# Kernel tuning notes

Measured on AMD Instinct MI355X. Metric: run time of the kernel, lower is better.

Reference implementation:

```python
import jax, jax.numpy as jnp
import numpy as np

T = 10
EPS = 1e-05
NUM_CHANNELS = 64  # d: whitening block size per group


def setup_inputs() -> dict:
    key = jax.random.key(0)
    X = jax.random.normal(key, (64, 256, 56, 56), dtype=jnp.float32)
    weight = jnp.ones((1, 256, 1, 1), dtype=jnp.float32)
    bias = jnp.zeros((1, 256, 1, 1), dtype=jnp.float32)
    return {"X": X, "weight": weight, "bias": bias}


def reference(X, weight, bias):
    N, C, H, W = X.shape
    d = NUM_CHANNELS
    g = C // d
    # [N,C,H,W] -> [C,N,H,W] -> (g, d, m)
    x = jnp.transpose(X, (1, 0, 2, 3)).reshape(g, d, -1)
    m = x.shape[-1]
    mean = jnp.mean(x, axis=-1, keepdims=True)          # (g, d, 1)
    xc = x - mean
    I = jnp.eye(d, dtype=X.dtype)
    # Sigma = eps*I + xc xc^T / m
    Sigma = EPS * I + jnp.einsum('gdm,gem->gde', xc, xc) / m
    rTr = 1.0 / jnp.trace(Sigma, axis1=1, axis2=2)[:, None, None]  # (g,1,1)
    Sigma_N = Sigma * rTr
    P0 = jnp.broadcast_to(I, (g, d, d))

    def newton_step(P, _):
        P3 = jnp.matmul(jnp.matmul(P, P), P)
        return 1.5 * P - 0.5 * jnp.matmul(P3, Sigma_N), None

    P, _ = jax.lax.scan(newton_step, P0, None, length=T)
    wm = P * jnp.sqrt(rTr)                               # (g, d, d)
    xn = jnp.matmul(wm, xc)                              # (g, d, m)
    X_hat = jnp.transpose(xn.reshape(C, N, H, W), (1, 0, 2, 3))
    return X_hat * weight + bias
```

## Files before the change

kernel.cpp:

```cpp
#include <hip/hip_runtime.h>


#define HWSZ 3136
#define CCH 256
#define DCH 64
#define MTOT (64 * HWSZ)
#define EPSV 1e-5f
#define TST 68
#define NST 68

typedef __attribute__((ext_vector_type(8))) short short8v;
typedef __attribute__((ext_vector_type(4))) float floatx4;

union F8U {
  short8v v;
  unsigned u[4];
  uint2 u2[2];
};

__device__ __forceinline__ unsigned short f2bf(float f) {
  unsigned u = __float_as_uint(f);
  u += 0x7fffu + ((u >> 16) & 1u);
  return (unsigned short)(u >> 16);
}
__device__ __forceinline__ float bf2f(unsigned short h) {
  return __uint_as_float(((unsigned)h) << 16);
}

__device__ __forceinline__ void sync_lds() {
  asm volatile("s_waitcnt lgkmcnt(0)\n\ts_barrier" ::: "memory");
}

__global__ __launch_bounds__(256) void cov_kernel(const float* __restrict__ X,
                                                  float* __restrict__ cov_dst,
                                                  float* __restrict__ sum_dst, int use_part) {
  __shared__ unsigned short tile[64 * TST];
  int bid = blockIdx.x;
  int g = bid >> 8;
  int nn = (bid >> 2) & 63;
  int qh = bid & 3;
  int ks0 = (qh * 49) >> 2;
  int ks1 = ((qh + 1) * 49) >> 2;
  int tid = threadIdx.x;
  int c = tid >> 2, q = tid & 3;
  int w = tid >> 6, lane = tid & 63, quad = lane >> 4, lm = lane & 15;

  floatx4 acc[4];
#pragma unroll
  for (int tj = 0; tj < 4; tj++) {
    floatx4 z = {0.f, 0.f, 0.f, 0.f};
    acc[tj] = z;
  }
  float fsum = 0.f;

  const float* xbase = X + ((size_t)(nn * CCH + g * DCH + c)) * HWSZ;

  float4 v[4];
  {
    int k0 = ks0 * 64;
#pragma unroll
    for (int j = 0; j < 4; j++) v[j] = *(const float4*)(xbase + k0 + j * 16 + q * 4);
  }

  for (int ks = ks0; ks < ks1; ks++) {
#pragma unroll
    for (int j = 0; j < 4; j++) {
      float4 t = v[j];
      fsum += t.x + t.y + t.z + t.w;
      unsigned d0 = (unsigned)f2bf(t.x) | ((unsigned)f2bf(t.y) << 16);
      unsigned d1 = (unsigned)f2bf(t.z) | ((unsigned)f2bf(t.w) << 16);
      *(uint2*)&tile[c * TST + j * 16 + q * 4] = make_uint2(d0, d1);
    }
    sync_lds();
    if (ks + 1 < ks1) {
      int k0 = (ks + 1) * 64;
#pragma unroll
      for (int j = 0; j < 4; j++) v[j] = *(const float4*)(xbase + k0 + j * 16 + q * 4);
    }
#pragma unroll
    for (int kk = 0; kk < 2; kk++) {
      F8U a;
      a.u2[0] = *(const uint2*)&tile[(16 * w + lm) * TST + kk * 32 + quad * 8];
      a.u2[1] = *(const uint2*)&tile[(16 * w + lm) * TST + kk * 32 + quad * 8 + 4];
#pragma unroll
      for (int tj = 0; tj < 4; tj++) {
        F8U b;
        b.u2[0] = *(const uint2*)&tile[(16 * tj + lm) * TST + kk * 32 + quad * 8];
        b.u2[1] = *(const uint2*)&tile[(16 * tj + lm) * TST + kk * 32 + quad * 8 + 4];
        acc[tj] = __builtin_amdgcn_mfma_f32_16x16x32_bf16(a.v, b.v, acc[tj], 0, 0, 0);
      }
    }
    sync_lds();
  }

  int pidx = bid & 255;
  if (use_part) {
    float* dst = cov_dst + ((size_t)g * 256 + pidx) * 4096;
#pragma unroll
    for (int tj = 0; tj < 4; tj++)
#pragma unroll
      for (int rr = 0; rr < 4; rr++)
        dst[(16 * w + quad * 4 + rr) * 64 + 16 * tj + lm] = acc[tj][rr];
  } else {
    float* dst = cov_dst + (size_t)g * 4096;
#pragma unroll
    for (int tj = 0; tj < 4; tj++)
#pragma unroll
      for (int rr = 0; rr < 4; rr++)
        atomicAdd(&dst[(16 * w + quad * 4 + rr) * 64 + 16 * tj + lm], acc[tj][rr]);
  }

  fsum += __shfl_xor(fsum, 1);
  fsum += __shfl_xor(fsum, 2);
  if (q == 0) {
    if (use_part)
      sum_dst[((size_t)g * 256 + pidx) * 64 + c] = fsum;
    else
      atomicAdd(&sum_dst[g * 64 + c], fsum);
  }
}

__global__ __launch_bounds__(256) void mean_kernel(const float* __restrict__ sum_part,
                                                   float* __restrict__ meanWS, int npart) {
  __shared__ float red[256];
  int g = blockIdx.x, tid = threadIdx.x;
  int c = tid & 63, p0 = tid >> 6;
  float s0 = 0.f, s1 = 0.f;
  for (int p = p0; p + 4 < npart; p += 8) {
    s0 += sum_part[((size_t)g * npart + p) * 64 + c];
    s1 += sum_part[((size_t)g * npart + p + 4) * 64 + c];
  }
  for (int p = p0 + ((npart - p0 + 7) / 8) * 8 - 8 + 8; p < npart; p += 4) s0 += 0.f;
  if (((npart >> 2) & 1) && (p0 + ((npart >> 2) - 1) * 4 < npart)) {
    int p = ((npart >> 2) - 1) * 4 + p0;
    if (p < npart) s0 += sum_part[((size_t)g * npart + p) * 64 + c];
  }
  red[tid] = s0 + s1;
  __syncthreads();
  if (tid < 64)
    meanWS[g * 64 + tid] =
        (red[tid] + red[tid + 64] + red[tid + 128] + red[tid + 192]) / (float)MTOT;
}

__global__ __launch_bounds__(256) void sigma_kernel(const float* __restrict__ cov_part,
                                                    const float* __restrict__ meanWS,
                                                    float* __restrict__ Sigma, int npart) {
  __shared__ float red[256];
  int b = blockIdx.x;
  int g = b >> 6, r = b & 63;
  int tid = threadIdx.x;
  int e = tid & 63, p0 = tid >> 6;
  float s = 0.f;
  for (int p = p0; p < npart; p += 4)
    s += cov_part[((size_t)g * npart + p) * 4096 + r * 64 + e];
  red[tid] = s;
  __syncthreads();
  if (tid < 64) {
    float tot = red[tid] + red[tid + 64] + red[tid + 128] + red[tid + 192];
    float mr = meanWS[g * 64 + r], me = meanWS[g * 64 + tid];
    Sigma[(size_t)g * 4096 + r * 64 + tid] =
        tot / (float)MTOT - mr * me + (r == tid ? EPSV : 0.f);
  }
}

__device__ __forceinline__ void mm_planes(floatx4 acc[4], const unsigned short* Ah,
                                          const unsigned short* Al, const unsigned short* Bh,
                                          const unsigned short* Bl, int w, int quad, int lm) {
#pragma unroll
  for (int tj = 0; tj < 4; tj++) {
    floatx4 z = {0.f, 0.f, 0.f, 0.f};
    acc[tj] = z;
  }
#pragma unroll
  for (int kk = 0; kk < 2; kk++) {
    int abase = (16 * w + lm) * NST + kk * 32 + quad * 8;
    F8U ahi, alo;
    ahi.u2[0] = *(const uint2*)&Ah[abase];
    ahi.u2[1] = *(const uint2*)&Ah[abase + 4];
    alo.u2[0] = *(const uint2*)&Al[abase];
    alo.u2[1] = *(const uint2*)&Al[abase + 4];
#pragma unroll
    for (int tj = 0; tj < 4; tj++) {
      int bbase = (16 * tj + lm) * NST + kk * 32 + quad * 8;
      F8U bhi, blo;
      bhi.u2[0] = *(const uint2*)&Bh[bbase];
      bhi.u2[1] = *(const uint2*)&Bh[bbase + 4];
      blo.u2[0] = *(const uint2*)&Bl[bbase];
      blo.u2[1] = *(const uint2*)&Bl[bbase + 4];
      acc[tj] = __builtin_amdgcn_mfma_f32_16x16x32_bf16(ahi.v, bhi.v, acc[tj], 0, 0, 0);
      acc[tj] = __builtin_amdgcn_mfma_f32_16x16x32_bf16(ahi.v, blo.v, acc[tj], 0, 0, 0);
      acc[tj] = __builtin_amdgcn_mfma_f32_16x16x32_bf16(alo.v, bhi.v, acc[tj], 0, 0, 0);
    }
  }
}

__device__ __forceinline__ void store_tr(const floatx4 acc[4], unsigned short* H,
                                         unsigned short* L, int w, int quad, int lm) {
#pragma unroll
  for (int tj = 0; tj < 4; tj++) {
    unsigned short hs[4], ls[4];
#pragma unroll
    for (int rr = 0; rr < 4; rr++) {
      float f = acc[tj][rr];
      hs[rr] = f2bf(f);
      ls[rr] = f2bf(f - bf2f(hs[rr]));
    }
    int a = (16 * tj + lm) * NST + 16 * w + quad * 4;
    *(uint2*)&H[a] = make_uint2((unsigned)hs[0] | ((unsigned)hs[1] << 16),
                                (unsigned)hs[2] | ((unsigned)hs[3] << 16));
    *(uint2*)&L[a] = make_uint2((unsigned)ls[0] | ((unsigned)ls[1] << 16),
                                (unsigned)ls[2] | ((unsigned)ls[3] << 16));
  }
}

__global__ __launch_bounds__(256) void newton_kernel(const float* __restrict__ Sigma,
                                                     unsigned short* __restrict__ wmB) {
  __shared__ unsigned short Ph[64 * NST], Pl[64 * NST];
  __shared__ unsigned short Sh[64 * NST], Sl[64 * NST];
  __shared__ unsigned short Th[64 * NST], Tl[64 * NST];
  __shared__ unsigned short Uh[64 * NST], Ul[64 * NST];
  __shared__ float diag[64];
  int g = blockIdx.x, tid = threadIdx.x;
  int w = tid >> 6, lane = tid & 63, quad = lane >> 4, lm = lane & 15;
  const float* Sg = Sigma + (size_t)g * 4096;

  if (tid < 64) diag[tid] = Sg[tid * 65];
  __syncthreads();
  float tr = 0.f;
#pragma unroll 8
  for (int i = 0; i < 64; i++) tr += diag[i];
  float rTr = 1.0f / tr;

  for (int idx = tid; idx < 4096; idx += 256) {
    int r = idx >> 6, c2 = idx & 63;
    float vv = Sg[idx] * rTr;
    unsigned short h = f2bf(vv);
    Sh[r * NST + c2] = h;
    Sl[r * NST + c2] = f2bf(vv - bf2f(h));
    Ph[r * NST + c2] = (r == c2) ? (unsigned short)0x3f80 : (unsigned short)0;
    Pl[r * NST + c2] = 0;
  }
  sync_lds();

  floatx4 acc[4];
  float pf[4][4];

  for (int t = 0; t < 10; t++) {
    mm_planes(acc, Ph, Pl, Ph, Pl, w, quad, lm);
    store_tr(acc, Th, Tl, w, quad, lm);
    sync_lds();
    mm_planes(acc, Th, Tl, Ph, Pl, w, quad, lm);
    store_tr(acc, Uh, Ul, w, quad, lm);
    sync_lds();
    mm_planes(acc, Uh, Ul, Sh, Sl, w, quad, lm);
#pragma unroll
    for (int tj = 0; tj < 4; tj++) {
      int a = (16 * tj + lm) * NST + 16 * w + quad * 4;
      uint2 ho = *(const uint2*)&Ph[a];
      uint2 lo = *(const uint2*)&Pl[a];
      unsigned short hs[4] = {(unsigned short)(ho.x & 0xffff), (unsigned short)(ho.x >> 16),
                              (unsigned short)(ho.y & 0xffff), (unsigned short)(ho.y >> 16)};
      unsigned short lss[4] = {(unsigned short)(lo.x & 0xffff), (unsigned short)(lo.x >> 16),
                               (unsigned short)(lo.y & 0xffff), (unsigned short)(lo.y >> 16)};
      unsigned short nh[4], nl[4];
#pragma unroll
      for (int rr = 0; rr < 4; rr++) {
        float pown = bf2f(hs[rr]) + bf2f(lss[rr]);
        float f = 1.5f * pown - 0.5f * acc[tj][rr];
        pf[tj][rr] = f;
        nh[rr] = f2bf(f);
        nl[rr] = f2bf(f - bf2f(nh[rr]));
      }
      *(uint2*)&Ph[a] = make_uint2((unsigned)nh[0] | ((unsigned)nh[1] << 16),
                                   (unsigned)nh[2] | ((unsigned)nh[3] << 16));
      *(uint2*)&Pl[a] = make_uint2((unsigned)nl[0] | ((unsigned)nl[1] << 16),
                                   (unsigned)nl[2] | ((unsigned)nl[3] << 16));
    }
    sync_lds();
  }

  float sc = sqrtf(rTr);
  unsigned short* wg = wmB + (size_t)g * 4096;
#pragma unroll
  for (int tj = 0; tj < 4; tj++)
#pragma unroll
    for (int rr = 0; rr < 4; rr++) {
      int row = 16 * w + quad * 4 + rr, col = 16 * tj + lm;
      wg[row * 64 + col] = f2bf(pf[tj][rr] * sc);
    }
}

__global__ __launch_bounds__(256) void apply_kernel(
    const float* __restrict__ X, const unsigned short* __restrict__ wmB,
    const float* __restrict__ meanWS, const float* __restrict__ weight,
    const float* __restrict__ bias, float* __restrict__ out) {
  __shared__ unsigned short T[64 * TST];
  __shared__ float meanv[64], wv[64], bv[64];
  int bid = blockIdx.x;
  int g = bid >> 8;
  int nn = (bid >> 2) & 63;
  int qh = bid & 3;
  int ks0 = (qh * 49) >> 2;
  int ks1 = ((qh + 1) * 49) >> 2;
  int tid = threadIdx.x;
  int w = tid >> 6, lane = tid & 63, quad = lane >> 4, lm = lane & 15;
  int sl = tid & 63;
  int cg = tid >> 6;

  if (tid < 64) {
    meanv[tid] = meanWS[g * 64 + tid];
    wv[tid] = weight[g * 64 + tid];
    bv[tid] = bias[g * 64 + tid];
  }
  F8U afrag[2];
#pragma unroll
  for (int kk = 0; kk < 2; kk++) {
    const uint2* p =
        (const uint2*)&wmB[(size_t)g * 4096 + (16 * w + lm) * 64 + kk * 32 + quad * 8];
    afrag[kk].u2[0] = p[0];
    afrag[kk].u2[1] = p[1];
  }
  __syncthreads();

  const float* xg = X + ((size_t)(nn * CCH + g * DCH)) * HWSZ;
  float* og = out + ((size_t)(nn * CCH + g * DCH)) * HWSZ;
  const float* xs = xg + (size_t)(cg * 16) * HWSZ + sl;

  float vv[16];
  {
    int k0 = ks0 * 64;
#pragma unroll
    for (int jp = 0; jp < 16; jp++) vv[jp] = xs[(size_t)jp * HWSZ + k0];
  }

  for (int ks = ks0; ks < ks1; ks++) {
    int k0 = ks * 64;
#pragma unroll
    for (int p2 = 0; p2 < 4; p2++) {
      unsigned d0 = (unsigned)f2bf(vv[4 * p2] - meanv[cg * 16 + 4 * p2]) |
                    ((unsigned)f2bf(vv[4 * p2 + 1] - meanv[cg * 16 + 4 * p2 + 1]) << 16);
      unsigned d1 = (unsigned)f2bf(vv[4 * p2 + 2] - meanv[cg * 16 + 4 * p2 + 2]) |
                    ((unsigned)f2bf(vv[4 * p2 + 3] - meanv[cg * 16 + 4 * p2 + 3]) << 16);
      *(uint2*)&T[sl * TST + cg * 16 + p2 * 4] = make_uint2(d0, d1);
    }
    sync_lds();
    if (ks + 1 < ks1) {
      int k0n = (ks + 1) * 64;
#pragma unroll
      for (int jp = 0; jp < 16; jp++) vv[jp] = xs[(size_t)jp * HWSZ + k0n];
    }
    floatx4 acc[4];
#pragma unroll
    for (int tj = 0; tj < 4; tj++) {
      floatx4 z = {0.f, 0.f, 0.f, 0.f};
      acc[tj] = z;
    }
#pragma unroll
    for (int kk = 0; kk < 2; kk++) {
#pragma unroll
      for (int tj = 0; tj < 4; tj++) {
        F8U b;
        b.u2[0] = *(const uint2*)&T[(16 * tj + lm) * TST + kk * 32 + quad * 8];
        b.u2[1] = *(const uint2*)&T[(16 * tj + lm) * TST + kk * 32 + quad * 8 + 4];
        acc[tj] = __builtin_amdgcn_mfma_f32_16x16x32_bf16(afrag[kk].v, b.v, acc[tj], 0, 0, 0);
      }
    }
#pragma unroll
    for (int tj = 0; tj < 4; tj++)
#pragma unroll
      for (int rr = 0; rr < 4; rr++) {
        int cc = 16 * w + quad * 4 + rr;
        og[(size_t)cc * HWSZ + k0 + 16 * tj + lm] = acc[tj][rr] * wv[cc] + bv[cc];
      }
    sync_lds();
  }
}

extern "C" void kernel_launch(void* const* d_in, const int* in_sizes, int n_in, void* d_out,
                              int out_size, void* d_ws, size_t ws_size, hipStream_t stream) {
  (void)in_sizes;
  (void)n_in;
  (void)out_size;
  const float* X = (const float*)d_in[0];
  const float* weight = (const float*)d_in[1];
  const float* bias = (const float*)d_in[2];
  float* out = (float*)d_out;
  char* ws = (char*)d_ws;

  float* Sigma = (float*)(ws + 0);
  float* meanWS = (float*)(ws + 65536);
  unsigned short* wmB = (unsigned short*)(ws + 66560);
  float* cov_dst = (float*)(ws + 99328);
  const size_t need_part = 99328u + 16777216u + 262144u;
  int use_part = (ws_size >= need_part) ? 1 : 0;
  float* sum_dst =
      use_part ? (float*)(ws + 99328 + 16777216) : (float*)(ws + 99328 + 65536);
  int npart = use_part ? 256 : 1;

  if (!use_part) {
    hipMemsetAsync(cov_dst, 0, 65536 + 1024, stream);
  }

  cov_kernel<<<dim3(1024), dim3(256), 0, stream>>>(X, cov_dst, sum_dst, use_part);
  mean_kernel<<<dim3(4), dim3(256), 0, stream>>>(sum_dst, meanWS, npart);
  sigma_kernel<<<dim3(256), dim3(256), 0, stream>>>(cov_dst, meanWS, Sigma, npart);
  newton_kernel<<<dim3(4), dim3(256), 0, stream>>>(Sigma, wmB);
  apply_kernel<<<dim3(1024), dim3(256), 0, stream>>>(X, wmB, meanWS, weight, bias, out);
}
```

Measured before the change: 453.6 us.

## Double-buffer LDS tiles, fuse mean into sigma kernel, widen Newton to 512 threads

The cov and apply kernels now use two LDS tile buffers, so each k-step needs one barrier instead of two and the next global load is issued before that barrier. The mean reduction moves into sigma_kernel, where every block recomputes the group mean from the partial sums; this removes one launch. The Newton kernel runs 8 waves, each computing half the column tiles, so the serial 64x64 iteration has more parallelism per block. The costs are double the LDS footprint and redundant mean reads in every sigma block.

```diff
diff --git a/kernel.cpp b/kernel.cpp
--- a/kernel.cpp
+++ b/kernel.cpp
@@ -34,7 +34,7 @@
 __global__ __launch_bounds__(256) void cov_kernel(const float* __restrict__ X,
                                                   float* __restrict__ cov_dst,
                                                   float* __restrict__ sum_dst, int use_part) {
-  __shared__ unsigned short tile[64 * TST];
+  __shared__ unsigned short tile[2][64 * TST];
   int bid = blockIdx.x;
   int g = bid >> 8;
   int nn = (bid >> 2) & 63;
@@ -62,6 +62,7 @@
     for (int j = 0; j < 4; j++) v[j] = *(const float4*)(xbase + k0 + j * 16 + q * 4);
   }
 
+  int p = 0;
   for (int ks = ks0; ks < ks1; ks++) {
 #pragma unroll
     for (int j = 0; j < 4; j++) {
@@ -69,28 +70,28 @@
       fsum += t.x + t.y + t.z + t.w;
       unsigned d0 = (unsigned)f2bf(t.x) | ((unsigned)f2bf(t.y) << 16);
       unsigned d1 = (unsigned)f2bf(t.z) | ((unsigned)f2bf(t.w) << 16);
-      *(uint2*)&tile[c * TST + j * 16 + q * 4] = make_uint2(d0, d1);
-    }
-    sync_lds();
+      *(uint2*)&tile[p][c * TST + j * 16 + q * 4] = make_uint2(d0, d1);
+    }
     if (ks + 1 < ks1) {
       int k0 = (ks + 1) * 64;
 #pragma unroll
       for (int j = 0; j < 4; j++) v[j] = *(const float4*)(xbase + k0 + j * 16 + q * 4);
     }
+    sync_lds();
 #pragma unroll
     for (int kk = 0; kk < 2; kk++) {
       F8U a;
-      a.u2[0] = *(const uint2*)&tile[(16 * w + lm) * TST + kk * 32 + quad * 8];
-      a.u2[1] = *(const uint2*)&tile[(16 * w + lm) * TST + kk * 32 + quad * 8 + 4];
+      a.u2[0] = *(const uint2*)&tile[p][(16 * w + lm) * TST + kk * 32 + quad * 8];
+      a.u2[1] = *(const uint2*)&tile[p][(16 * w + lm) * TST + kk * 32 + quad * 8 + 4];
 #pragma unroll
       for (int tj = 0; tj < 4; tj++) {
         F8U b;
-        b.u2[0] = *(const uint2*)&tile[(16 * tj + lm) * TST + kk * 32 + quad * 8];
-        b.u2[1] = *(const uint2*)&tile[(16 * tj + lm) * TST + kk * 32 + quad * 8 + 4];
+        b.u2[0] = *(const uint2*)&tile[p][(16 * tj + lm) * TST + kk * 32 + quad * 8];
+        b.u2[1] = *(const uint2*)&tile[p][(16 * tj + lm) * TST + kk * 32 + quad * 8 + 4];
         acc[tj] = __builtin_amdgcn_mfma_f32_16x16x32_bf16(a.v, b.v, acc[tj], 0, 0, 0);
       }
     }
-    sync_lds();
+    p ^= 1;
   }
 
   int pidx = bid & 255;
@@ -120,68 +121,60 @@
   }
 }
 
-__global__ __launch_bounds__(256) void mean_kernel(const float* __restrict__ sum_part,
-                                                   float* __restrict__ meanWS, int npart) {
+__global__ __launch_bounds__(256) void sigma_kernel(const float* __restrict__ cov_part,
+                                                    const float* __restrict__ sum_part,
+                                                    float* __restrict__ Sigma,
+                                                    float* __restrict__ meanWS, int npart) {
   __shared__ float red[256];
-  int g = blockIdx.x, tid = threadIdx.x;
-  int c = tid & 63, p0 = tid >> 6;
-  float s0 = 0.f, s1 = 0.f;
-  for (int p = p0; p + 4 < npart; p += 8) {
-    s0 += sum_part[((size_t)g * npart + p) * 64 + c];
-    s1 += sum_part[((size_t)g * npart + p + 4) * 64 + c];
-  }
-  for (int p = p0 + ((npart - p0 + 7) / 8) * 8 - 8 + 8; p < npart; p += 4) s0 += 0.f;
-  if (((npart >> 2) & 1) && (p0 + ((npart >> 2) - 1) * 4 < npart)) {
-    int p = ((npart >> 2) - 1) * 4 + p0;
-    if (p < npart) s0 += sum_part[((size_t)g * npart + p) * 64 + c];
-  }
-  red[tid] = s0 + s1;
-  __syncthreads();
-  if (tid < 64)
-    meanWS[g * 64 + tid] =
-        (red[tid] + red[tid + 64] + red[tid + 128] + red[tid + 192]) / (float)MTOT;
-}
-
-__global__ __launch_bounds__(256) void sigma_kernel(const float* __restrict__ cov_part,
-                                                    const float* __restrict__ meanWS,
-                                                    float* __restrict__ Sigma, int npart) {
-  __shared__ float red[256];
+  __shared__ float meanv[64];
   int b = blockIdx.x;
   int g = b >> 6, r = b & 63;
   int tid = threadIdx.x;
-  int e = tid & 63, p0 = tid >> 6;
+  int c = tid & 63, p0 = tid >> 6;
+
   float s = 0.f;
-  for (int p = p0; p < npart; p += 4)
-    s += cov_part[((size_t)g * npart + p) * 4096 + r * 64 + e];
+  for (int pp = p0; pp < npart; pp += 4)
+    s += sum_part[((size_t)g * npart + pp) * 64 + c];
   red[tid] = s;
+  __syncthreads();
+  if (tid < 64)
+    meanv[tid] = (red[tid] + red[tid + 64] + red[tid + 128] + red[tid + 192]) / (float)MTOT;
+
+  float s2 = 0.f;
+  for (int pp = p0; pp < npart; pp += 4)
+    s2 += cov_part[((size_t)g * npart + pp) * 4096 + r * 64 + c];
+  __syncthreads();
+  red[tid] = s2;
   __syncthreads();
   if (tid < 64) {
     float tot = red[tid] + red[tid + 64] + red[tid + 128] + red[tid + 192];
-    float mr = meanWS[g * 64 + r], me = meanWS[g * 64 + tid];
     Sigma[(size_t)g * 4096 + r * 64 + tid] =
-        tot / (float)MTOT - mr * me + (r == tid ? EPSV : 0.f);
-  }
-}
-
-__device__ __forceinline__ void mm_planes(floatx4 acc[4], const unsigned short* Ah,
+        tot / (float)MTOT - meanv[r] * meanv[tid] + (r == tid ? EPSV : 0.f);
+    if (r == 0) meanWS[g * 64 + tid] = meanv[tid];
+  }
+}
+
+__device__ __forceinline__ void mm_planes(floatx4 acc[2], const unsigned short* Ah,
                                           const unsigned short* Al, const unsigned short* Bh,
-                                          const unsigned short* Bl, int w, int quad, int lm) {
-#pragma unroll
-  for (int tj = 0; tj < 4; tj++) {
+                                          const unsigned short* Bl, int rw, int ch, int quad,
+                                          int lm) {
+#pragma unroll
+  for (int tj = 0; tj < 2; tj++) {
     floatx4 z = {0.f, 0.f, 0.f, 0.f};
     acc[tj] = z;
   }
 #pragma unroll
   for (int kk = 0; kk < 2; kk++) {
-    int abase = (16 * w + lm) * NST + kk * 32 + quad * 8;
+    int abase = (16 * rw + lm) * NST + kk * 32 + quad * 8;
     F8U ahi, alo;
     ahi.u2[0] = *(const uint2*)&Ah[abase];
     ahi.u2[1] = *(const uint2*)&Ah[abase + 4];
     alo.u2[0] = *(const uint2*)&Al[abase];
     alo.u2[1] = *(const uint2*)&Al[abase + 4];
 #pragma unroll
-    for (int tj = 0; tj < 4; tj++) {
-      int bbase = (16 * tj + lm) * NST + kk * 32 + quad * 8;
+    for (int tj = 0; tj < 2; tj++) {
+      int tjg = 2 * ch + tj;
+      int bbase = (16 * tjg + lm) * NST + kk * 32 + quad * 8;
       F8U bhi, blo;
       bhi.u2[0] = *(const uint2*)&Bh[bbase];
       bhi.u2[1] = *(const uint2*)&Bh[bbase + 4];
@@ -194,10 +187,11 @@
   }
 }
 
-__device__ __forceinline__ void store_tr(const floatx4 acc[4], unsigned short* H,
-                                         unsigned short* L, int w, int quad, int lm) {
-#pragma unroll
-  for (int tj = 0; tj < 4; tj++) {
+__device__ __forceinline__ void store_tr(const floatx4 acc[2], unsigned short* H,
+                                         unsigned short* L, int rw, int ch, int quad, int lm) {
+#pragma unroll
+  for (int tj = 0; tj < 2; tj++) {
+    int tjg = 2 * ch + tj;
     unsigned short hs[4], ls[4];
 #pragma unroll
     for (int rr = 0; rr < 4; rr++) {
@@ -205,7 +199,7 @@
       hs[rr] = f2bf(f);
       ls[rr] = f2bf(f - bf2f(hs[rr]));
     }
-    int a = (16 * tj + lm) * NST + 16 * w + quad * 4;
+    int a = (16 * tjg + lm) * NST + 16 * rw + quad * 4;
     *(uint2*)&H[a] = make_uint2((unsigned)hs[0] | ((unsigned)hs[1] << 16),
                                 (unsigned)hs[2] | ((unsigned)hs[3] << 16));
     *(uint2*)&L[a] = make_uint2((unsigned)ls[0] | ((unsigned)ls[1] << 16),
@@ -213,7 +207,7 @@
   }
 }
 
-__global__ __launch_bounds__(256) void newton_kernel(const float* __restrict__ Sigma,
+__global__ __launch_bounds__(512) void newton_kernel(const float* __restrict__ Sigma,
                                                      unsigned short* __restrict__ wmB) {
   __shared__ unsigned short Ph[64 * NST], Pl[64 * NST];
   __shared__ unsigned short Sh[64 * NST], Sl[64 * NST];
@@ -222,6 +216,7 @@
   __shared__ float diag[64];
   int g = blockIdx.x, tid = threadIdx.x;
   int w = tid >> 6, lane = tid & 63, quad = lane >> 4, lm = lane & 15;
+  int rw = w & 3, ch = w >> 2;
   const float* Sg = Sigma + (size_t)g * 4096;
 
   if (tid < 64) diag[tid] = Sg[tid * 65];
@@ -231,7 +226,7 @@
   for (int i = 0; i < 64; i++) tr += diag[i];
   float rTr = 1.0f / tr;
 
-  for (int idx = tid; idx < 4096; idx += 256) {
+  for (int idx = tid; idx < 4096; idx += 512) {
     int r = idx >> 6, c2 = idx & 63;
     float vv = Sg[idx] * rTr;
     unsigned short h = f2bf(vv);
@@ -242,20 +237,21 @@
   }
   sync_lds();
 
-  floatx4 acc[4];
-  float pf[4][4];
+  floatx4 acc[2];
+  float pf[2][4];
 
   for (int t = 0; t < 10; t++) {
-    mm_planes(acc, Ph, Pl, Ph, Pl, w, quad, lm);
-    store_tr(acc, Th, Tl, w, quad, lm);
+    mm_planes(acc, Ph, Pl, Ph, Pl, rw, ch, quad, lm);
+    store_tr(acc, Th, Tl, rw, ch, quad, lm);
     sync_lds();
-    mm_planes(acc, Th, Tl, Ph, Pl, w, quad, lm);
-    store_tr(acc, Uh, Ul, w, quad, lm);
+    mm_planes(acc, Th, Tl, Ph, Pl, rw, ch, quad, lm);
+    store_tr(acc, Uh, Ul, rw, ch, quad, lm);
     sync_lds();
-    mm_planes(acc, Uh, Ul, Sh, Sl, w, quad, lm);
-#pragma unroll
-    for (int tj = 0; tj < 4; tj++) {
-      int a = (16 * tj + lm) * NST + 16 * w + quad * 4;
+    mm_planes(acc, Uh, Ul, Sh, Sl, rw, ch, quad, lm);
+#pragma unroll
+    for (int tj = 0; tj < 2; tj++) {
+      int tjg = 2 * ch + tj;
+      int a = (16 * tjg + lm) * NST + 16 * rw + quad * 4;
       uint2 ho = *(const uint2*)&Ph[a];
       uint2 lo = *(const uint2*)&Pl[a];
       unsigned short hs[4] = {(unsigned short)(ho.x & 0xffff), (unsigned short)(ho.x >> 16),
@@ -282,10 +278,10 @@
   float sc = sqrtf(rTr);
   unsigned short* wg = wmB + (size_t)g * 4096;
 #pragma unroll
-  for (int tj = 0; tj < 4; tj++)
+  for (int tj = 0; tj < 2; tj++)
 #pragma unroll
     for (int rr = 0; rr < 4; rr++) {
-      int row = 16 * w + quad * 4 + rr, col = 16 * tj + lm;
+      int row = 16 * rw + quad * 4 + rr, col = 16 * (2 * ch + tj) + lm;
       wg[row * 64 + col] = f2bf(pf[tj][rr] * sc);
     }
 }
@@ -294,7 +290,7 @@
     const float* __restrict__ X, const unsigned short* __restrict__ wmB,
     const float* __restrict__ meanWS, const float* __restrict__ weight,
     const float* __restrict__ bias, float* __restrict__ out) {
-  __shared__ unsigned short T[64 * TST];
+  __shared__ unsigned short T[2][64 * TST];
   __shared__ float meanv[64], wv[64], bv[64];
   int bid = blockIdx.x;
   int g = bid >> 8;
@@ -333,6 +329,7 @@
     for (int jp = 0; jp < 16; jp++) vv[jp] = xs[(size_t)jp * HWSZ + k0];
   }
 
+  int p = 0;
   for (int ks = ks0; ks < ks1; ks++) {
     int k0 = ks * 64;
 #pragma unroll
@@ -341,14 +338,14 @@
                     ((unsigned)f2bf(vv[4 * p2 + 1] - meanv[cg * 16 + 4 * p2 + 1]) << 16);
       unsigned d1 = (unsigned)f2bf(vv[4 * p2 + 2] - meanv[cg * 16 + 4 * p2 + 2]) |
                     ((unsigned)f2bf(vv[4 * p2 + 3] - meanv[cg * 16 + 4 * p2 + 3]) << 16);
-      *(uint2*)&T[sl * TST + cg * 16 + p2 * 4] = make_uint2(d0, d1);
-    }
-    sync_lds();
+      *(uint2*)&T[p][sl * TST + cg * 16 + p2 * 4] = make_uint2(d0, d1);
+    }
     if (ks + 1 < ks1) {
       int k0n = (ks + 1) * 64;
 #pragma unroll
       for (int jp = 0; jp < 16; jp++) vv[jp] = xs[(size_t)jp * HWSZ + k0n];
     }
+    sync_lds();
     floatx4 acc[4];
 #pragma unroll
     for (int tj = 0; tj < 4; tj++) {
@@ -360,8 +357,8 @@
 #pragma unroll
       for (int tj = 0; tj < 4; tj++) {
         F8U b;
-        b.u2[0] = *(const uint2*)&T[(16 * tj + lm) * TST + kk * 32 + quad * 8];
-        b.u2[1] = *(const uint2*)&T[(16 * tj + lm) * TST + kk * 32 + quad * 8 + 4];
+        b.u2[0] = *(const uint2*)&T[p][(16 * tj + lm) * TST + kk * 32 + quad * 8];
+        b.u2[1] = *(const uint2*)&T[p][(16 * tj + lm) * TST + kk * 32 + quad * 8 + 4];
         acc[tj] = __builtin_amdgcn_mfma_f32_16x16x32_bf16(afrag[kk].v, b.v, acc[tj], 0, 0, 0);
       }
     }
@@ -372,7 +369,7 @@
         int cc = 16 * w + quad * 4 + rr;
         og[(size_t)cc * HWSZ + k0 + 16 * tj + lm] = acc[tj][rr] * wv[cc] + bv[cc];
       }
-    sync_lds();
+    p ^= 1;
   }
 }
 
@@ -402,8 +399,7 @@
   }
 
   cov_kernel<<<dim3(1024), dim3(256), 0, stream>>>(X, cov_dst, sum_dst, use_part);
-  mean_kernel<<<dim3(4), dim3(256), 0, stream>>>(sum_dst, meanWS, npart);
-  sigma_kernel<<<dim3(256), dim3(256), 0, stream>>>(cov_dst, meanWS, Sigma, npart);
-  newton_kernel<<<dim3(4), dim3(256), 0, stream>>>(Sigma, wmB);
+  sigma_kernel<<<dim3(256), dim3(256), 0, stream>>>(cov_dst, sum_dst, Sigma, meanWS, npart);
+  newton_kernel<<<dim3(4), dim3(512), 0, stream>>>(Sigma, wmB);
   apply_kernel<<<dim3(1024), dim3(256), 0, stream>>>(X, wmB, meanWS, weight, bias, out);
 }
```

After: 455.8 us. No clear change (+0.5%).
